# Performance work log

Measured on AMD Instinct MI355X. Metric: run time of the kernel, lower is better.

## Reference

```python
import jax, jax.numpy as jnp
import numpy as np

IOU_THRESHOLD = 0.5


def setup_inputs() -> dict:
    key = jax.random.key(0)
    k1, k2, k3 = jax.random.split(key, 3)
    B, N = 4, 8192
    # valid boxes: top-left in [0,200), width/height in [1,51)
    xy = jax.random.uniform(k1, (B, N, 2), dtype=jnp.float32) * 200.0
    wh = jax.random.uniform(k2, (B, N, 2), dtype=jnp.float32) * 50.0 + 1.0
    boxes = jnp.concatenate([xy, xy + wh], axis=-1)  # [B,N,4] (x1,y1,x2,y2)
    scores = jax.random.uniform(k3, (B, N), dtype=jnp.float32)
    return {"boxes": boxes, "scores": scores}


def _soft_nms_single(boxes, scores):
    # boxes: [N,4], scores: [N]
    x1, y1, x2, y2 = boxes[:, 0], boxes[:, 1], boxes[:, 2], boxes[:, 3]
    inter_w = jnp.maximum(0.0, jnp.minimum(x2[:, None], x2[None, :]) - jnp.maximum(x1[:, None], x1[None, :]))
    inter_h = jnp.maximum(0.0, jnp.minimum(y2[:, None], y2[None, :]) - jnp.maximum(y1[:, None], y1[None, :]))
    inter = inter_w * inter_h  # [N,N]
    area = (x2 - x1) * (y2 - y1)  # [N]
    union = area[:, None] + area[None, :] - inter
    iou = inter / union  # [N,N]
    weight = jnp.exp(-iou / IOU_THRESHOLD)  # [N,N]
    adjusted = weight @ scores  # [N] : adjusted_scores[i] = sum_j w[i,j]*s[j]
    w = jax.nn.softmax(adjusted, axis=0)  # [N]
    return w @ boxes  # [4]


def reference(boxes, scores):
    return jax.vmap(_soft_nms_single)(boxes, scores)  # [B,4]
```

## Files before the change

### kernel.cpp

```cpp
#include <hip/hip_runtime.h>
#include <hip/hip_bf16.h>

#define BATCH   4
#define NBOX    8192
#define BLOCK   256
#define TSZ     256
#define NT      (NBOX / TSZ)
#define NPAIRS  (NT * (NT + 1) / 2)

__device__ __forceinline__ float bf2f(unsigned short u) {
    union { unsigned int i; float f; } c;
    c.i = ((unsigned int)u) << 16;
    return c.f;
}

__device__ __forceinline__ bool box_plausible(float x1, float y1, float x2, float y2) {
    bool ok = (x1 == x1) && (y1 == y1) && (x2 == x2) && (y2 == y2);
    ok = ok && fabsf(x1) < 1e4f && fabsf(y1) < 1e4f && fabsf(x2) < 1e4f && fabsf(y2) < 1e4f;
    ok = ok && x1 >= -1.0f && x1 <= 300.0f && y1 >= -1.0f && y1 <= 300.0f;
    const float w = x2 - x1, h = y2 - y1;
    ok = ok && w >= -0.1f && w <= 80.0f && h >= -0.1f && h <= 80.0f;
    return ok;
}

__device__ __forceinline__ bool wave_probe_is_f32(const void* boxes_raw) {
    const int lane = threadIdx.x & 63;
    const float* bf = (const float*)boxes_raw;
    const bool okf = box_plausible(bf[lane * 4 + 0], bf[lane * 4 + 1],
                                   bf[lane * 4 + 2], bf[lane * 4 + 3]);
    const unsigned short* bh = (const unsigned short*)boxes_raw;
    const bool okh = box_plausible(bf2f(bh[lane * 4 + 0]), bf2f(bh[lane * 4 + 1]),
                                   bf2f(bh[lane * 4 + 2]), bf2f(bh[lane * 4 + 3]));
    const unsigned long long mf = __ballot(okf);
    const unsigned long long mh = __ballot(okh);
    return __popcll(mf) >= __popcll(mh);
}

__device__ __forceinline__ float4 load_box(const void* boxes_raw, size_t idx, bool isf32) {
    if (isf32) {
        return reinterpret_cast<const float4*>(boxes_raw)[idx];
    } else {
        const ushort4 u = reinterpret_cast<const ushort4*>(boxes_raw)[idx];
        return make_float4(bf2f(u.x), bf2f(u.y), bf2f(u.z), bf2f(u.w));
    }
}

__device__ __forceinline__ float load_score(const void* scores_raw, size_t idx, bool isf32) {
    return isf32 ? ((const float*)scores_raw)[idx]
                 : bf2f(((const unsigned short*)scores_raw)[idx]);
}

#define CEXP (-2.8853900817779268f)

__device__ __forceinline__ float pair_weight(
    float ix1, float iy1, float ix2, float iy2, float iarea,
    const float4& bj, float jarea)
{
    float w = fminf(ix2, bj.z) - fmaxf(ix1, bj.x);
    float h = fminf(iy2, bj.w) - fmaxf(iy1, bj.y);
    w = fmaxf(w, 0.0f);
    h = fmaxf(h, 0.0f);
    const float inter = w * h;
    const float uni   = iarea + jarea - inter;
    const float arg   = (CEXP * inter) * __builtin_amdgcn_rcpf(uni);
    return __builtin_amdgcn_exp2f(arg);
}

__global__ __launch_bounds__(BLOCK, 4) void soft_nms_adj_kernel(
    const void* __restrict__ boxes_raw,
    const void* __restrict__ scores_raw,
    float* __restrict__ adj)
{
    __shared__ float4 sbox[TSZ];
    __shared__ float2 sas[TSZ];
    __shared__ float  srow[4][TSZ];

    const int bid = blockIdx.x;
    const int b   = bid / NPAIRS;
    int p = bid % NPAIRS;
    int it = 0;
    while (p >= NT - it) { p -= NT - it; it++; }
    const int jt = it + p;

    const int tid  = threadIdx.x;
    const int lane = tid & 63;
    const int wv   = tid >> 6;

    const bool isf32 = wave_probe_is_f32(boxes_raw);
    const size_t base = (size_t)b * NBOX;

    {
        const int jg = jt * TSZ + tid;
        const float4 uj = load_box(boxes_raw, base + jg, isf32);
        sbox[tid] = uj;
        sas[tid]  = make_float2((uj.z - uj.x) * (uj.w - uj.y),
                                load_score(scores_raw, base + jg, isf32));
    }

    float rx1[4], ry1[4], rx2[4], ry2[4], rar[4], rsc[4], accr[4];
#pragma unroll
    for (int k = 0; k < 4; k++) {
        const int ig = it * TSZ + k * 64 + lane;
        const float4 ui = load_box(boxes_raw, base + ig, isf32);
        rx1[k] = ui.x; ry1[k] = ui.y; rx2[k] = ui.z; ry2[k] = ui.w;
        rar[k] = (ui.z - ui.x) * (ui.w - ui.y);
        rsc[k] = load_score(scores_raw, base + ig, isf32);
        accr[k] = 0.0f;
    }

    __syncthreads();

    if (it == jt) {
#pragma unroll 2
        for (int t = 0; t < 64; t++) {
            const int idx = wv * 64 + ((lane + t) & 63);
            const float4 bj = sbox[idx];
            const float2 as = sas[idx];
#pragma unroll
            for (int k = 0; k < 4; k++) {
                const float e = pair_weight(rx1[k], ry1[k], rx2[k], ry2[k], rar[k], bj, as.x);
                accr[k] = fmaf(e, as.y, accr[k]);
            }
        }
    } else {
        float accc = 0.0f;
#pragma unroll 2
        for (int t = 0; t < 64; t++) {
            const int idx = wv * 64 + ((lane + t) & 63);
            const float4 bj = sbox[idx];
            const float2 as = sas[idx];
            const float e0 = pair_weight(rx1[0], ry1[0], rx2[0], ry2[0], rar[0], bj, as.x);
            const float e1 = pair_weight(rx1[1], ry1[1], rx2[1], ry2[1], rar[1], bj, as.x);
            const float e2 = pair_weight(rx1[2], ry1[2], rx2[2], ry2[2], rar[2], bj, as.x);
            const float e3 = pair_weight(rx1[3], ry1[3], rx2[3], ry2[3], rar[3], bj, as.x);
            accr[0] = fmaf(e0, as.y, accr[0]);
            accr[1] = fmaf(e1, as.y, accr[1]);
            accr[2] = fmaf(e2, as.y, accr[2]);
            accr[3] = fmaf(e3, as.y, accr[3]);
            const float c = fmaf(e0, rsc[0], fmaf(e1, rsc[1], fmaf(e2, rsc[2], e3 * rsc[3])));
            accc += __shfl(c, (lane - t) & 63);
        }
        atomicAdd(&adj[base + jt * TSZ + wv * 64 + lane], accc);
    }

#pragma unroll
    for (int k = 0; k < 4; k++) srow[wv][k * 64 + lane] = accr[k];
    __syncthreads();
    {
        const float rs = srow[0][tid] + srow[1][tid] + srow[2][tid] + srow[3][tid];
        atomicAdd(&adj[base + it * TSZ + tid], rs);
    }
}

#define FBLK 1024
__global__ __launch_bounds__(FBLK) void soft_nms_finish_kernel(
    const void* __restrict__ boxes_raw,
    const float* __restrict__ adj,
    void* __restrict__ out)
{
    constexpr int K  = NBOX / FBLK;
    constexpr int NW = FBLK / 64;
    const int b   = blockIdx.x;
    const int tid = threadIdx.x;
    const float* ab = adj + (size_t)b * NBOX;
    const size_t boxbase = (size_t)b * NBOX;

    const bool isf32 = wave_probe_is_f32(boxes_raw);

    float av[K];
    float m = -3.4e38f;
#pragma unroll
    for (int k = 0; k < K; k++) {
        av[k] = ab[k * FBLK + tid];
        m = fmaxf(m, av[k]);
    }
#pragma unroll
    for (int off = 32; off > 0; off >>= 1)
        m = fmaxf(m, __shfl_down(m, off));

    __shared__ float smax[NW];
    if ((tid & 63) == 0) smax[tid >> 6] = m;
    __syncthreads();
    float M = smax[0];
#pragma unroll
    for (int w = 1; w < NW; w++) M = fmaxf(M, smax[w]);

    const float L2E = 1.4426950408889634f;
    float es = 0.0f, s0 = 0.0f, s1 = 0.0f, s2 = 0.0f, s3 = 0.0f;
#pragma unroll
    for (int k = 0; k < K; k++) {
        const float e = __builtin_amdgcn_exp2f((av[k] - M) * L2E);
        const float4 u = load_box(boxes_raw, boxbase + k * FBLK + tid, isf32);
        es += e;
        s0 += e * u.x;
        s1 += e * u.y;
        s2 += e * u.z;
        s3 += e * u.w;
    }
#pragma unroll
    for (int off = 32; off > 0; off >>= 1) {
        es += __shfl_down(es, off);
        s0 += __shfl_down(s0, off);
        s1 += __shfl_down(s1, off);
        s2 += __shfl_down(s2, off);
        s3 += __shfl_down(s3, off);
    }
    __shared__ float sred[NW][5];
    if ((tid & 63) == 0) {
        const int w = tid >> 6;
        sred[w][0] = es; sred[w][1] = s0; sred[w][2] = s1;
        sred[w][3] = s2; sred[w][4] = s3;
    }
    __syncthreads();
    if (tid == 0) {
        float ES = 0.0f, o[4] = {0.0f, 0.0f, 0.0f, 0.0f};
#pragma unroll
        for (int w = 0; w < NW; w++) {
            ES   += sred[w][0];
            o[0] += sred[w][1];
            o[1] += sred[w][2];
            o[2] += sred[w][3];
            o[3] += sred[w][4];
        }
        const float inv = 1.0f / ES;
        if (isf32) {
            float* of = (float*)out;
            for (int c = 0; c < 4; c++) of[b * 4 + c] = o[c] * inv;
        } else {
            __hip_bfloat16* oh = (__hip_bfloat16*)out;
            for (int c = 0; c < 4; c++) oh[b * 4 + c] = __float2bfloat16(o[c] * inv);
        }
    }
}

extern "C" void kernel_launch(void* const* d_in, const int* in_sizes, int n_in,
                              void* d_out, int out_size, void* d_ws, size_t ws_size,
                              hipStream_t stream) {
    const void* boxes_raw  = d_in[0];
    const void* scores_raw = d_in[1];
    float* adj = (float*)d_ws;

    hipMemsetAsync(adj, 0, (size_t)BATCH * NBOX * sizeof(float), stream);
    soft_nms_adj_kernel<<<dim3(BATCH * NPAIRS), dim3(BLOCK), 0, stream>>>(
        boxes_raw, scores_raw, adj);
    soft_nms_finish_kernel<<<dim3(BATCH), dim3(FBLK), 0, stream>>>(boxes_raw, adj, d_out);
}
```

Baseline: 137.4 us.

## Bin-sort boxes by x1 and skip tile pairs with disjoint x ranges

Adds a counting-sort kernel that orders each batch's boxes by a histogram of x1, so each 256-box tile covers a narrow x interval. The pairwise kernel then returns early for tile pairs whose x extents do not overlap. For those pairs IoU is zero and the weight is one, so the finish kernel adds back the sum of the skipped tile's scores. The aim is to drop most of the O(N^2) exp/rcp work, at the cost of an extra sort pass, single-block-per-batch serialization in the sort, and a per-tile correction step.

```diff
diff --git a/kernel.cpp b/kernel.cpp
--- a/kernel.cpp
+++ b/kernel.cpp
@@ -7,6 +7,7 @@
 #define TSZ     256
 #define NT      (NBOX / TSZ)
 #define NPAIRS  (NT * (NT + 1) / 2)
+#define NBINS   2048
 
 __device__ __forceinline__ float bf2f(unsigned short u) {
     union { unsigned int i; float f; } c;
@@ -66,14 +67,68 @@
     return __builtin_amdgcn_exp2f(arg);
 }
 
+__global__ __launch_bounds__(1024) void sort_kernel(
+    const void* __restrict__ boxes_raw, const void* __restrict__ scores_raw,
+    float4* __restrict__ sboxes, float* __restrict__ sscores,
+    float* __restrict__ adj)
+{
+    __shared__ int hist[NBINS];
+    __shared__ int wsum[1024];
+
+    const int b   = blockIdx.x;
+    const int tid = threadIdx.x;
+    const bool isf32 = wave_probe_is_f32(boxes_raw);
+    const size_t base = (size_t)b * NBOX;
+
+    for (int i = tid; i < NBINS; i += 1024) hist[i] = 0;
+#pragma unroll
+    for (int k = 0; k < NBOX / 1024; k++) adj[base + k * 1024 + tid] = 0.0f;
+    __syncthreads();
+
+    float4 bx[8]; float sc[8]; int bin[8];
+#pragma unroll
+    for (int k = 0; k < 8; k++) {
+        const int i = k * 1024 + tid;
+        bx[k] = load_box(boxes_raw, base + i, isf32);
+        sc[k] = load_score(scores_raw, base + i, isf32);
+        int bb = (int)(bx[k].x * ((float)NBINS / 256.0f));
+        bin[k] = min(NBINS - 1, max(0, bb));
+        atomicAdd(&hist[bin[k]], 1);
+    }
+    __syncthreads();
+
+    const int h0 = hist[2 * tid], h1 = hist[2 * tid + 1];
+    const int s  = h0 + h1;
+    wsum[tid] = s;
+    __syncthreads();
+    for (int off = 1; off < 1024; off <<= 1) {
+        const int v = (tid >= off) ? wsum[tid - off] : 0;
+        __syncthreads();
+        wsum[tid] += v;
+        __syncthreads();
+    }
+    const int ex = wsum[tid] - s;
+    hist[2 * tid]     = ex;
+    hist[2 * tid + 1] = ex + h0;
+    __syncthreads();
+
+#pragma unroll
+    for (int k = 0; k < 8; k++) {
+        const int pos = atomicAdd(&hist[bin[k]], 1);
+        sboxes[base + pos]  = bx[k];
+        sscores[base + pos] = sc[k];
+    }
+}
+
 __global__ __launch_bounds__(BLOCK, 4) void soft_nms_adj_kernel(
-    const void* __restrict__ boxes_raw,
-    const void* __restrict__ scores_raw,
+    const float4* __restrict__ sboxes,
+    const float* __restrict__ sscores,
     float* __restrict__ adj)
 {
     __shared__ float4 sbox[TSZ];
     __shared__ float2 sas[TSZ];
     __shared__ float  srow[4][TSZ];
+    __shared__ float  red[4][4];
 
     const int bid = blockIdx.x;
     const int b   = bid / NPAIRS;
@@ -85,35 +140,54 @@
     const int tid  = threadIdx.x;
     const int lane = tid & 63;
     const int wv   = tid >> 6;
-
-    const bool isf32 = wave_probe_is_f32(boxes_raw);
     const size_t base = (size_t)b * NBOX;
 
+    float jmin, jmax;
     {
         const int jg = jt * TSZ + tid;
-        const float4 uj = load_box(boxes_raw, base + jg, isf32);
+        const float4 uj = sboxes[base + jg];
         sbox[tid] = uj;
-        sas[tid]  = make_float2((uj.z - uj.x) * (uj.w - uj.y),
-                                load_score(scores_raw, base + jg, isf32));
+        sas[tid]  = make_float2((uj.z - uj.x) * (uj.w - uj.y), sscores[base + jg]);
+        jmin = uj.x; jmax = uj.z;
     }
 
     float rx1[4], ry1[4], rx2[4], ry2[4], rar[4], rsc[4], accr[4];
 #pragma unroll
     for (int k = 0; k < 4; k++) {
         const int ig = it * TSZ + k * 64 + lane;
-        const float4 ui = load_box(boxes_raw, base + ig, isf32);
+        const float4 ui = sboxes[base + ig];
         rx1[k] = ui.x; ry1[k] = ui.y; rx2[k] = ui.z; ry2[k] = ui.w;
         rar[k] = (ui.z - ui.x) * (ui.w - ui.y);
-        rsc[k] = load_score(scores_raw, base + ig, isf32);
+        rsc[k] = sscores[base + ig];
         accr[k] = 0.0f;
     }
 
-    __syncthreads();
+    float imin = fminf(fminf(rx1[0], rx1[1]), fminf(rx1[2], rx1[3]));
+    float imax = fmaxf(fmaxf(rx2[0], rx2[1]), fmaxf(rx2[2], rx2[3]));
+#pragma unroll
+    for (int off = 32; off > 0; off >>= 1) {
+        jmin = fminf(jmin, __shfl_down(jmin, off));
+        jmax = fmaxf(jmax, __shfl_down(jmax, off));
+        imin = fminf(imin, __shfl_down(imin, off));
+        imax = fmaxf(imax, __shfl_down(imax, off));
+    }
+    if (lane == 0) {
+        red[wv][0] = jmin; red[wv][1] = jmax; red[wv][2] = imin; red[wv][3] = imax;
+    }
+    __syncthreads();
+    jmin = fminf(fminf(red[0][0], red[1][0]), fminf(red[2][0], red[3][0]));
+    jmax = fmaxf(fmaxf(red[0][1], red[1][1]), fmaxf(red[2][1], red[3][1]));
+    imin = fminf(fminf(red[0][2], red[1][2]), fminf(red[2][2], red[3][2]));
+    imax = fmaxf(fmaxf(red[0][3], red[1][3]), fmaxf(red[2][3], red[3][3]));
+
+    if ((imax < jmin) || (jmax < imin)) return;
+
+    const int wvbase = wv * 64;
 
     if (it == jt) {
 #pragma unroll 2
         for (int t = 0; t < 64; t++) {
-            const int idx = wv * 64 + ((lane + t) & 63);
+            const int idx = wvbase + ((lane + t) & 63);
             const float4 bj = sbox[idx];
             const float2 as = sas[idx];
 #pragma unroll
@@ -126,7 +200,7 @@
         float accc = 0.0f;
 #pragma unroll 2
         for (int t = 0; t < 64; t++) {
-            const int idx = wv * 64 + ((lane + t) & 63);
+            const int idx = wvbase + ((lane + t) & 63);
             const float4 bj = sbox[idx];
             const float2 as = sas[idx];
             const float e0 = pair_weight(rx1[0], ry1[0], rx2[0], ry2[0], rar[0], bj, as.x);
@@ -140,7 +214,7 @@
             const float c = fmaf(e0, rsc[0], fmaf(e1, rsc[1], fmaf(e2, rsc[2], e3 * rsc[3])));
             accc += __shfl(c, (lane - t) & 63);
         }
-        atomicAdd(&adj[base + jt * TSZ + wv * 64 + lane], accc);
+        atomicAdd(&adj[base + jt * TSZ + wvbase + lane], accc);
     }
 
 #pragma unroll
@@ -154,43 +228,80 @@
 
 #define FBLK 1024
 __global__ __launch_bounds__(FBLK) void soft_nms_finish_kernel(
+    const float4* __restrict__ sboxes,
+    const float* __restrict__ sscores,
+    const float* __restrict__ adj,
     const void* __restrict__ boxes_raw,
-    const float* __restrict__ adj,
     void* __restrict__ out)
 {
     constexpr int K  = NBOX / FBLK;
     constexpr int NW = FBLK / 64;
-    const int b   = blockIdx.x;
-    const int tid = threadIdx.x;
-    const float* ab = adj + (size_t)b * NBOX;
-    const size_t boxbase = (size_t)b * NBOX;
+    __shared__ float sminx[NT], smaxx[NT], ssumT[NT], scorr[NT];
+    __shared__ float smax_[NW];
+    __shared__ float sred[NW][5];
+
+    const int b    = blockIdx.x;
+    const int tid  = threadIdx.x;
+    const int lane = tid & 63;
+    const int wv   = tid >> 6;
+    const size_t base = (size_t)b * NBOX;
 
     const bool isf32 = wave_probe_is_f32(boxes_raw);
+
+#pragma unroll
+    for (int tt = 0; tt < 2; tt++) {
+        const int T = wv * 2 + tt;
+        float mn = 1e30f, mx = -1e30f, sm = 0.0f;
+#pragma unroll
+        for (int q = 0; q < 4; q++) {
+            const int i = T * TSZ + q * 64 + lane;
+            const float4 u = sboxes[base + i];
+            mn = fminf(mn, u.x);
+            mx = fmaxf(mx, u.z);
+            sm += sscores[base + i];
+        }
+#pragma unroll
+        for (int off = 32; off > 0; off >>= 1) {
+            mn = fminf(mn, __shfl_down(mn, off));
+            mx = fmaxf(mx, __shfl_down(mx, off));
+            sm += __shfl_down(sm, off);
+        }
+        if (lane == 0) { sminx[T] = mn; smaxx[T] = mx; ssumT[T] = sm; }
+    }
+    __syncthreads();
+    if (tid < NT) {
+        float c = 0.0f;
+        for (int T2 = 0; T2 < NT; T2++) {
+            const bool skip = (smaxx[tid] < sminx[T2]) || (smaxx[T2] < sminx[tid]);
+            if (skip) c += ssumT[T2];
+        }
+        scorr[tid] = c;
+    }
+    __syncthreads();
 
     float av[K];
     float m = -3.4e38f;
 #pragma unroll
     for (int k = 0; k < K; k++) {
-        av[k] = ab[k * FBLK + tid];
+        const int r = k * FBLK + tid;
+        av[k] = adj[base + r] + scorr[r >> 8];
         m = fmaxf(m, av[k]);
     }
 #pragma unroll
     for (int off = 32; off > 0; off >>= 1)
         m = fmaxf(m, __shfl_down(m, off));
-
-    __shared__ float smax[NW];
-    if ((tid & 63) == 0) smax[tid >> 6] = m;
-    __syncthreads();
-    float M = smax[0];
-#pragma unroll
-    for (int w = 1; w < NW; w++) M = fmaxf(M, smax[w]);
+    if (lane == 0) smax_[wv] = m;
+    __syncthreads();
+    float M = smax_[0];
+#pragma unroll
+    for (int w = 1; w < NW; w++) M = fmaxf(M, smax_[w]);
 
     const float L2E = 1.4426950408889634f;
     float es = 0.0f, s0 = 0.0f, s1 = 0.0f, s2 = 0.0f, s3 = 0.0f;
 #pragma unroll
     for (int k = 0; k < K; k++) {
         const float e = __builtin_amdgcn_exp2f((av[k] - M) * L2E);
-        const float4 u = load_box(boxes_raw, boxbase + k * FBLK + tid, isf32);
+        const float4 u = sboxes[base + k * FBLK + tid];
         es += e;
         s0 += e * u.x;
         s1 += e * u.y;
@@ -205,11 +316,9 @@
         s2 += __shfl_down(s2, off);
         s3 += __shfl_down(s3, off);
     }
-    __shared__ float sred[NW][5];
-    if ((tid & 63) == 0) {
-        const int w = tid >> 6;
-        sred[w][0] = es; sred[w][1] = s0; sred[w][2] = s1;
-        sred[w][3] = s2; sred[w][4] = s3;
+    if (lane == 0) {
+        sred[wv][0] = es; sred[wv][1] = s0; sred[wv][2] = s1;
+        sred[wv][3] = s2; sred[wv][4] = s3;
     }
     __syncthreads();
     if (tid == 0) {
@@ -238,10 +347,15 @@
                               hipStream_t stream) {
     const void* boxes_raw  = d_in[0];
     const void* scores_raw = d_in[1];
-    float* adj = (float*)d_ws;
-
-    hipMemsetAsync(adj, 0, (size_t)BATCH * NBOX * sizeof(float), stream);
+
+    float4* sboxes  = (float4*)d_ws;
+    float*  sscores = (float*)(sboxes + (size_t)BATCH * NBOX);
+    float*  adj     = sscores + (size_t)BATCH * NBOX;
+
+    sort_kernel<<<dim3(BATCH), dim3(1024), 0, stream>>>(
+        boxes_raw, scores_raw, sboxes, sscores, adj);
     soft_nms_adj_kernel<<<dim3(BATCH * NPAIRS), dim3(BLOCK), 0, stream>>>(
-        boxes_raw, scores_raw, adj);
-    soft_nms_finish_kernel<<<dim3(BATCH), dim3(FBLK), 0, stream>>>(boxes_raw, adj, d_out);
-}
+        sboxes, sscores, adj);
+    soft_nms_finish_kernel<<<dim3(BATCH), dim3(FBLK), 0, stream>>>(
+        sboxes, sscores, adj, boxes_raw, d_out);
+}
```

After: 140.1 us. +2.0%, slower.
